# Kernel tuning notes

Hardware: AMD Instinct MI355X
Metric: run time of the kernel (lower is better)

## Reference

```python
import jax, jax.numpy as jnp
import numpy as np

DIM = 2048
N_HEADS = 32
N_KV_HEADS = 8
HEAD_DIM = 64
BATCH = 2
SEQ = 2048
N_REP = N_HEADS // N_KV_HEADS
SCALE = HEAD_DIM ** -0.5
ROPE_BASE = 10000.0


def setup_inputs() -> dict:
    key = jax.random.key(0)
    ks = jax.random.split(key, 5)
    x = jax.random.normal(ks[0], (BATCH, SEQ, DIM), dtype=jnp.float32)
    # weights stored as (in, out) so projection is x @ W
    Wq = jax.random.normal(ks[1], (DIM, N_HEADS * HEAD_DIM), dtype=jnp.float32) * (DIM ** -0.5)
    Wk = jax.random.normal(ks[2], (DIM, N_KV_HEADS * HEAD_DIM), dtype=jnp.float32) * (DIM ** -0.5)
    Wv = jax.random.normal(ks[3], (DIM, N_KV_HEADS * HEAD_DIM), dtype=jnp.float32) * (DIM ** -0.5)
    Wo = jax.random.normal(ks[4], (N_HEADS * HEAD_DIM, DIM), dtype=jnp.float32) * ((N_HEADS * HEAD_DIM) ** -0.5)
    # RoPE tables (seq, head_dim)
    inv_freq = 1.0 / (ROPE_BASE ** (jnp.arange(0, HEAD_DIM, 2, dtype=jnp.float32) / HEAD_DIM))
    t = jnp.arange(SEQ, dtype=jnp.float32)
    freqs = jnp.outer(t, inv_freq)                      # (S, D/2)
    emb = jnp.concatenate([freqs, freqs], axis=-1)      # (S, D)
    cos = jnp.cos(emb)
    sin = jnp.sin(emb)
    # additive causal mask (1,1,S,S)
    neg = jnp.finfo(jnp.float32).min
    causal = jnp.tril(jnp.ones((SEQ, SEQ), dtype=bool))
    attention_mask = jnp.where(causal, 0.0, neg)[None, None, :, :].astype(jnp.float32)
    return {"x": x, "Wq": Wq, "Wk": Wk, "Wv": Wv, "Wo": Wo,
            "cos": cos, "sin": sin, "attention_mask": attention_mask}


def _rotate_half(u):
    h = u.shape[-1] // 2
    return jnp.concatenate([-u[..., h:], u[..., :h]], axis=-1)


def reference(x, Wq, Wk, Wv, Wo, cos, sin, attention_mask):
    b, s, _ = x.shape
    q = (x @ Wq).reshape(b, s, N_HEADS, HEAD_DIM)
    k = (x @ Wk).reshape(b, s, N_KV_HEADS, HEAD_DIM)
    v = (x @ Wv).reshape(b, s, N_KV_HEADS, HEAD_DIM)
    # RoPE, broadcast over head dim (unsqueeze_dim=2)
    c = cos[None, :, None, :]
    sn = sin[None, :, None, :]
    q = q * c + _rotate_half(q) * sn
    k = k * c + _rotate_half(k) * sn
    # repeat KV heads for GQA: (b,s,kvh,d) -> (b,s,h,d)
    k = jnp.repeat(k, N_REP, axis=2)
    v = jnp.repeat(v, N_REP, axis=2)
    # (b,h,s,d)
    q = q.transpose(0, 2, 1, 3)
    k = k.transpose(0, 2, 1, 3)
    v = v.transpose(0, 2, 1, 3)
    scores = jnp.einsum("bhqd,bhkd->bhqk", q, k) * SCALE + attention_mask
    attn = jax.nn.softmax(scores.astype(jnp.float32), axis=-1).astype(q.dtype)
    out = jnp.einsum("bhqk,bhkd->bhqd", attn, v)
    out = out.transpose(0, 2, 1, 3).reshape(b, s, N_HEADS * HEAD_DIM)
    return out @ Wo
```

## Files before the change

### kernel.cpp

```cpp
#include <hip/hip_runtime.h>
#include <hip/hip_bf16.h>

typedef unsigned short u16;
typedef unsigned int   u32;
typedef __bf16 bf16_t;
typedef bf16_t bf16x8 __attribute__((ext_vector_type(8)));
typedef u16    u16x8  __attribute__((ext_vector_type(8)));
typedef float  f32x4  __attribute__((ext_vector_type(4)));

#define DIM  2048
#define SEQ  2048
#define BATCH 2
#define NH   32
#define NKVH 8
#define HD   64
#define KVDIM (NKVH*HD)
#define NQKV (DIM + 2*KVDIM)
#define SCALE 0.125f

__device__ __forceinline__ float b2f(u16 u) {
  union { u32 i; float f; } v; v.i = ((u32)u) << 16; return v.f;
}
__device__ __forceinline__ u16 f2b(float f) {
  union { float f; u32 i; } v; v.f = f;
  u32 x = v.i;
  return (u16)((x + 0x7fffu + ((x >> 16) & 1u)) >> 16);
}
__device__ __forceinline__ u32 pkbf2(float a, float b) {
  __hip_bfloat162 h = __float22bfloat162_rn(float2{a, b});
  union { __hip_bfloat162 h; u32 u; } v; v.h = h; return v.u;
}
__device__ __forceinline__ int probe_bf16(const u32* probe) { return probe[0] != 0u; }
__device__ __forceinline__ float ext_ld(const void* p, long idx, int mode_bf16) {
  return mode_bf16 ? b2f(((const u16*)p)[idx]) : ((const float*)p)[idx];
}
__device__ __forceinline__ f32x4 ld4(const void* p, long idx, int mode_bf16) {
  f32x4 r;
  if (mode_bf16) {
    ushort4 v = *(const ushort4*)((const u16*)p + idx);
    r[0] = b2f(v.x); r[1] = b2f(v.y); r[2] = b2f(v.z); r[3] = b2f(v.w);
  } else {
    float4 v = *(const float4*)((const float*)p + idx);
    r[0] = v.x; r[1] = v.y; r[2] = v.z; r[3] = v.w;
  }
  return r;
}
__device__ __forceinline__ void gload_lds16(const u16* g, u16* l) {
  __builtin_amdgcn_global_load_lds((const __attribute__((address_space(1))) void*)g,
                                   (__attribute__((address_space(3))) void*)l, 16, 0, 0);
}

__global__ void prep(const void* __restrict__ Wq, const void* __restrict__ Wk,
                     const void* __restrict__ Wv, const void* __restrict__ Wo,
                     const void* __restrict__ x, u16* __restrict__ WqkvT,
                     u16* __restrict__ WoT, u16* __restrict__ xb, int use_xb,
                     const u32* __restrict__ probe) {
  int mode = probe_bf16(probe);
  int xt = blockIdx.x;
  int tx = threadIdx.x, ty = threadIdx.y;
  if (xt < 160) {
    __shared__ u16 t[32][33];
    const void* in; int C, c0, obase; u16* out; int ld;
    if (xt < 64)       { in = Wq; C = DIM;   c0 = xt * 32;        obase = 0;           out = WqkvT; ld = DIM; }
    else if (xt < 80)  { in = Wk; C = KVDIM; c0 = (xt - 64) * 32; obase = DIM;         out = WqkvT; ld = DIM; }
    else if (xt < 96)  { in = Wv; C = KVDIM; c0 = (xt - 80) * 32; obase = DIM + KVDIM; out = WqkvT; ld = DIM; }
    else               { in = Wo; C = DIM;   c0 = (xt - 96) * 32; obase = 0;           out = WoT;   ld = DIM; }
    int r0 = blockIdx.y * 32;
#pragma unroll
    for (int i = 0; i < 32; i += 8)
      t[ty + i][tx] = mode ? ((const u16*)in)[(long)(r0 + ty + i) * C + c0 + tx]
                           : f2b(((const float*)in)[(long)(r0 + ty + i) * C + c0 + tx]);
    __syncthreads();
#pragma unroll
    for (int i = 0; i < 32; i += 8)
      out[(long)(obase + c0 + ty + i) * ld + r0 + tx] = t[tx][ty + i];
  } else {
    if (mode || !use_xb) return;
    int tid = ty * 32 + tx;
    long base = ((long)((xt - 160) * 64 + blockIdx.y) * 256 + tid) * 8;
    float4 f0 = *(const float4*)((const float*)x + base);
    float4 f1 = *(const float4*)((const float*)x + base + 4);
    u16x8 t8;
    t8[0] = f2b(f0.x); t8[1] = f2b(f0.y); t8[2] = f2b(f0.z); t8[3] = f2b(f0.w);
    t8[4] = f2b(f1.x); t8[5] = f2b(f1.y); t8[6] = f2b(f1.z); t8[7] = f2b(f1.w);
    *(u16x8*)&xb[base] = t8;
  }
}


__launch_bounds__(256)
__global__ void gemm_qkv(const void* __restrict__ x, const u16* __restrict__ xb,
                         int use_xb, const u16* __restrict__ Bt,
                         u16* __restrict__ Qb, u16* __restrict__ Kb, u16* __restrict__ Vt,
                         const void* __restrict__ cosb, const void* __restrict__ sinb,
                         const u32* __restrict__ probe) {
  int pmode = probe_bf16(probe);
  int mode = (use_xb || pmode) ? 1 : 0;
  const u16* A16 = pmode ? (const u16*)x : xb;
  const float* Af = (const float*)x;
  __shared__ __align__(16) u16 As[128 * 32];
  __shared__ __align__(16) u16 Bs[128 * 32];
  int tid = threadIdx.x, lane = tid & 63, wv = tid >> 6;
  int l16 = lane & 15, q = lane >> 4;
  int bm0 = blockIdx.y * 128, bn0 = blockIdx.x * 128;
  int mbase = (wv & 1) * 64, nbase = (wv >> 1) * 64;
  int c0 = tid, c1 = tid + 256;
  int r0 = c0 >> 2, s0 = (c0 & 3) ^ ((r0 >> 1) & 3);
  int r1 = c1 >> 2, s1 = (c1 & 3) ^ ((r1 >> 1) & 3);
  const int K = DIM;
  long aoff0 = (long)(bm0 + r0) * K + s0 * 8;
  long aoff1 = (long)(bm0 + r1) * K + s1 * 8;
  long boff0 = (long)(bn0 + r0) * K + s0 * 8;
  long boff1 = (long)(bn0 + r1) * K + s1 * 8;
  int rsw = (q ^ ((l16 >> 1) & 3)) * 8;
  f32x4 acc[4][4] = {};

  for (int k0 = 0; k0 < K; k0 += 32) {
    __syncthreads();
    if (mode) {
      gload_lds16(A16 + aoff0 + k0, &As[wv * 512]);
      gload_lds16(A16 + aoff1 + k0, &As[2048 + wv * 512]);
    } else {
      float4 f0 = *(const float4*)(Af + aoff0 + k0);
      float4 f1 = *(const float4*)(Af + aoff0 + k0 + 4);
      u16x8 t;
      t[0] = f2b(f0.x); t[1] = f2b(f0.y); t[2] = f2b(f0.z); t[3] = f2b(f0.w);
      t[4] = f2b(f1.x); t[5] = f2b(f1.y); t[6] = f2b(f1.z); t[7] = f2b(f1.w);
      *(u16x8*)&As[c0 * 8] = t;
      float4 g0 = *(const float4*)(Af + aoff1 + k0);
      float4 g1 = *(const float4*)(Af + aoff1 + k0 + 4);
      u16x8 u;
      u[0] = f2b(g0.x); u[1] = f2b(g0.y); u[2] = f2b(g0.z); u[3] = f2b(g0.w);
      u[4] = f2b(g1.x); u[5] = f2b(g1.y); u[6] = f2b(g1.z); u[7] = f2b(g1.w);
      *(u16x8*)&As[c1 * 8] = u;
    }
    gload_lds16(Bt + boff0 + k0, &Bs[wv * 512]);
    gload_lds16(Bt + boff1 + k0, &Bs[2048 + wv * 512]);
    __syncthreads();
    bf16x8 af[4], bfr[4];
#pragma unroll
    for (int mi = 0; mi < 4; mi++)
      af[mi] = *(const bf16x8*)&As[(mbase + mi * 16 + l16) * 32 + rsw];
#pragma unroll
    for (int ni = 0; ni < 4; ni++)
      bfr[ni] = *(const bf16x8*)&Bs[(nbase + ni * 16 + l16) * 32 + rsw];
#pragma unroll
    for (int mi = 0; mi < 4; mi++)
#pragma unroll
      for (int ni = 0; ni < 4; ni++)
        acc[mi][ni] = __builtin_amdgcn_mfma_f32_16x16x32_bf16(
            bfr[ni], af[mi], acc[mi][ni], 0, 0, 0);
  }

  if (bn0 < DIM + KVDIM) {
    u16* Cb; int ldc, ncol0; float osc;
    if (bn0 < DIM) { Cb = Qb; ldc = DIM; ncol0 = bn0; osc = SCALE; }
    else           { Cb = Kb; ldc = KVDIM; ncol0 = bn0 - DIM; osc = 1.0f; }
#pragma unroll
    for (int mi = 0; mi < 4; mi++) {
      int m = bm0 + mbase + mi * 16 + l16;
      int st = m & (SEQ - 1);
#pragma unroll
      for (int ni = 0; ni < 2; ni++) {
        int dl = ni * 16 + q * 4;
        f32x4 c4 = ld4(cosb, (long)st * HD + dl, pmode);
        f32x4 s4 = ld4(sinb, (long)st * HD + dl, pmode);
        float lo[4], hi[4];
#pragma unroll
        for (int r = 0; r < 4; r++) {
          float a = acc[mi][ni][r], b = acc[mi][ni + 2][r];
          lo[r] = (a * c4[r] - b * s4[r]) * osc;
          hi[r] = (b * c4[r] + a * s4[r]) * osc;
        }
        int n0 = ncol0 + nbase + dl;
        uint2 w0, w1;
        w0.x = pkbf2(lo[0], lo[1]); w0.y = pkbf2(lo[2], lo[3]);
        w1.x = pkbf2(hi[0], hi[1]); w1.y = pkbf2(hi[2], hi[3]);
        *(uint2*)&Cb[(long)m * ldc + n0]      = w0;
        *(uint2*)&Cb[(long)m * ldc + n0 + 32] = w1;
      }
    }
  } else {
    int vcol0 = bn0 - DIM - KVDIM;
#pragma unroll
    for (int mi = 0; mi < 4; mi++) {
      int m = bm0 + mbase + mi * 16 + l16;
      int bb = m >> 11, s = m & (SEQ - 1);
#pragma unroll
      for (int ni = 0; ni < 4; ni++) {
        int vcol = vcol0 + nbase + ni * 16 + q * 4;
        int kvh2 = vcol >> 6, d = vcol & 63;
        long vb = ((long)(bb * NKVH + kvh2) * HD + d) * SEQ + s;
#pragma unroll
        for (int r = 0; r < 4; r++)
          Vt[vb + (long)r * SEQ] = f2b(acc[mi][ni][r]);
      }
    }
  }
}

__launch_bounds__(256)
__global__ void gemm_ao(const u16* __restrict__ A, const u16* __restrict__ Bt,
                        void* __restrict__ C, const u32* __restrict__ probe) {
  int mode = probe_bf16(probe);
  __shared__ __align__(16) u16 As[128 * 32];
  __shared__ __align__(16) u16 Bs[128 * 32];
  int tid = threadIdx.x, lane = tid & 63, wv = tid >> 6;
  int l16 = lane & 15, q = lane >> 4;
  int bm0 = blockIdx.y * 128, bn0 = blockIdx.x * 128;
  int mbase = (wv & 1) * 64, nbase = (wv >> 1) * 64;
  int c0 = tid, c1 = tid + 256;
  int r0 = c0 >> 2, s0 = (c0 & 3) ^ ((r0 >> 1) & 3);
  int r1 = c1 >> 2, s1 = (c1 & 3) ^ ((r1 >> 1) & 3);
  const int K = DIM;
  long aoff0 = (long)(bm0 + r0) * K + s0 * 8;
  long aoff1 = (long)(bm0 + r1) * K + s1 * 8;
  long boff0 = (long)(bn0 + r0) * K + s0 * 8;
  long boff1 = (long)(bn0 + r1) * K + s1 * 8;
  int rsw = (q ^ ((l16 >> 1) & 3)) * 8;
  f32x4 acc[4][4] = {};
  for (int k0 = 0; k0 < K; k0 += 32) {
    __syncthreads();
    gload_lds16(A + aoff0 + k0, &As[wv * 512]);
    gload_lds16(A + aoff1 + k0, &As[2048 + wv * 512]);
    gload_lds16(Bt + boff0 + k0, &Bs[wv * 512]);
    gload_lds16(Bt + boff1 + k0, &Bs[2048 + wv * 512]);
    __syncthreads();
    bf16x8 af[4], bfr[4];
#pragma unroll
    for (int mi = 0; mi < 4; mi++)
      af[mi] = *(const bf16x8*)&As[(mbase + mi * 16 + l16) * 32 + rsw];
#pragma unroll
    for (int ni = 0; ni < 4; ni++)
      bfr[ni] = *(const bf16x8*)&Bs[(nbase + ni * 16 + l16) * 32 + rsw];
#pragma unroll
    for (int mi = 0; mi < 4; mi++)
#pragma unroll
      for (int ni = 0; ni < 4; ni++)
        acc[mi][ni] = __builtin_amdgcn_mfma_f32_16x16x32_bf16(
            bfr[ni], af[mi], acc[mi][ni], 0, 0, 0);
  }
#pragma unroll
  for (int mi = 0; mi < 4; mi++)
#pragma unroll
    for (int ni = 0; ni < 4; ni++) {
      int m = bm0 + mbase + mi * 16 + l16;
      int n0 = bn0 + nbase + ni * 16 + q * 4;
      if (mode) {
        uint2 w;
        w.x = pkbf2(acc[mi][ni][0], acc[mi][ni][1]);
        w.y = pkbf2(acc[mi][ni][2], acc[mi][ni][3]);
        *(uint2*)&((u16*)C)[(long)m * DIM + n0] = w;
      } else {
        float4 f;
        f.x = acc[mi][ni][0]; f.y = acc[mi][ni][1];
        f.z = acc[mi][ni][2]; f.w = acc[mi][ni][3];
        *(float4*)&((float*)C)[(long)m * DIM + n0] = f;
      }
    }
}

__launch_bounds__(256, 2)
__global__ void attn_kernel(const u16* __restrict__ Q, const u16* __restrict__ K,
                            const u16* __restrict__ Vt, u16* __restrict__ AO) {
  __shared__ __align__(16) u16 Ks[2 * 64 * 64];
  __shared__ __align__(16) u16 Vs[2 * 64 * 64];
  __shared__ __align__(16) u16 Ps[4][32 * 64];
  int tid = threadIdx.x, lane = tid & 63, wv = tid >> 6;
  int l16 = lane & 15, q = lane >> 4;
  int i = blockIdx.x;
  int bh = blockIdx.y;
  int b = bh >> 5, h = bh & 31, kvh = h >> 2;
  const u16* Kp = K + (long)b * SEQ * KVDIM + kvh * HD;
  const u16* Vp = Vt + (long)(b * NKVH + kvh) * HD * SEQ;

  int cA = tid, cB = tid + 256;
  int rA = cA >> 3, bA = (cA & 7) ^ (rA & 7);
  int rB = cB >> 3, bB = (cB & 7) ^ (rB & 7);
  const u16* kSrcA = Kp + (long)rA * KVDIM + bA * 8;
  const u16* kSrcB = Kp + (long)rB * KVDIM + bB * 8;
  const u16* vSrcA = Vp + (long)rA * SEQ + bA * 8;
  const u16* vSrcB = Vp + (long)rB * SEQ + bB * 8;
  u16* kDstA = &Ks[(wv * 64 + lane) * 8];
  u16* kDstB = &Ks[(256 + wv * 64 + lane) * 8];
  u16* vDstA = &Vs[(wv * 64 + lane) * 8];
  u16* vDstB = &Vs[(256 + wv * 64 + lane) * 8];

  int e = l16 & 7;
  int off0 = (q ^ e) * 8;
  int off1 = ((4 + q) ^ e) * 8;

  bf16x8 ones;
#pragma unroll
  for (int j = 0; j < 8; j++) ones[j] = (bf16_t)1.0f;

#pragma unroll
  for (int ph = 0; ph < 2; ph++) {
    int t = ph ? (15 - i) : i;
    int qbase = t * 128 + wv * 32;
    const u16* Qp = Q + (long)(b * SEQ + qbase) * DIM + h * HD;
    bf16x8 aq[2][2];
#pragma unroll
    for (int qr = 0; qr < 2; qr++) {
      aq[qr][0] = *(const bf16x8*)&Qp[(qr * 16 + l16) * DIM + q * 8];
      aq[qr][1] = *(const bf16x8*)&Qp[(qr * 16 + l16) * DIM + 32 + q * 8];
    }
    f32x4 o_acc[2][4] = {};
    f32x4 l_acc[2] = {};
    int nkt = 2 * (t + 1);
    int wmax = qbase + 31;

    __syncthreads();
    gload_lds16(kSrcA, kDstA);
    gload_lds16(kSrcB, kDstB);
    gload_lds16(vSrcA, vDstA);
    gload_lds16(vSrcB, vDstB);
    int curo = 0;

    for (int kt = 0; kt < nkt; kt++) {
      __syncthreads();
      if (kt + 1 < nkt) {
        long kk2 = (long)(kt + 1) * 64;
        int nxt = curo ^ 4096;
        gload_lds16(kSrcA + kk2 * KVDIM, kDstA + nxt);
        gload_lds16(kSrcB + kk2 * KVDIM, kDstB + nxt);
        gload_lds16(vSrcA + kk2, vDstA + nxt);
        gload_lds16(vSrcB + kk2, vDstB + nxt);
      }
      int kk = kt * 64;
      if (kk > wmax) { curo ^= 4096; continue; }
      const u16* Ksb = &Ks[curo];
      const u16* Vsb = &Vs[curo];

      bf16x8 bk[4][2], bv[4][2];
#pragma unroll
      for (int ni = 0; ni < 4; ni++) {
        bk[ni][0] = *(const bf16x8*)&Ksb[(ni * 16 + l16) * 64 + off0];
        bk[ni][1] = *(const bf16x8*)&Ksb[(ni * 16 + l16) * 64 + off1];
      }
#pragma unroll
      for (int di = 0; di < 4; di++) {
        bv[di][0] = *(const bf16x8*)&Vsb[(di * 16 + l16) * 64 + off0];
        bv[di][1] = *(const bf16x8*)&Vsb[(di * 16 + l16) * 64 + off1];
      }
      bool diag = (kt >= 2 * t);
#pragma unroll
      for (int qr = 0; qr < 2; qr++) {
        int qb16 = qbase + qr * 16;
        if (kk > qb16 + 15) continue;
        f32x4 sc[4];
#pragma unroll
        for (int ni = 0; ni < 4; ni++) {
          f32x4 z = {};
          z = __builtin_amdgcn_mfma_f32_16x16x32_bf16(bk[ni][0], aq[qr][0], z, 0, 0, 0);
          z = __builtin_amdgcn_mfma_f32_16x16x32_bf16(bk[ni][1], aq[qr][1], z, 0, 0, 0);
          sc[ni] = z;
        }
        int qrow = qb16 + l16;
        if (diag) {
#pragma unroll
          for (int ni = 0; ni < 4; ni++)
#pragma unroll
            for (int r = 0; r < 4; r++) {
              int kv = kk + ni * 16 + q * 4 + r;
              float p = __expf(sc[ni][r]);
              sc[ni][r] = (kv <= qrow) ? p : 0.f;
            }
        } else {
#pragma unroll
          for (int ni = 0; ni < 4; ni++)
#pragma unroll
            for (int r = 0; r < 4; r++) sc[ni][r] = __expf(sc[ni][r]);
        }
#pragma unroll
        for (int ni = 0; ni < 4; ni++) {
          uint2 w;
          w.x = pkbf2(sc[ni][0], sc[ni][1]);
          w.y = pkbf2(sc[ni][2], sc[ni][3]);
          int pblk = (2 * ni + (q >> 1)) ^ e;
          *(uint2*)&Ps[wv][(qr * 16 + l16) * 64 + pblk * 8 + (q & 1) * 4] = w;
        }
        bf16x8 ap0 = *(const bf16x8*)&Ps[wv][(qr * 16 + l16) * 64 + off0];
        bf16x8 ap1 = *(const bf16x8*)&Ps[wv][(qr * 16 + l16) * 64 + off1];
        l_acc[qr] = __builtin_amdgcn_mfma_f32_16x16x32_bf16(ap0, ones, l_acc[qr], 0, 0, 0);
        l_acc[qr] = __builtin_amdgcn_mfma_f32_16x16x32_bf16(ap1, ones, l_acc[qr], 0, 0, 0);
#pragma unroll
        for (int di = 0; di < 4; di++) {
          o_acc[qr][di] = __builtin_amdgcn_mfma_f32_16x16x32_bf16(ap0, bv[di][0], o_acc[qr][di], 0, 0, 0);
          o_acc[qr][di] = __builtin_amdgcn_mfma_f32_16x16x32_bf16(ap1, bv[di][1], o_acc[qr][di], 0, 0, 0);
        }
      }
      curo ^= 4096;
    }
#pragma unroll
    for (int qr = 0; qr < 2; qr++) {
      long obase = (long)(b * SEQ + qbase + qr * 16 + q * 4) * DIM + h * HD;
#pragma unroll
      for (int r = 0; r < 4; r++) {
        float inv = 1.0f / l_acc[qr][r];
#pragma unroll
        for (int di = 0; di < 4; di++)
          AO[obase + (long)r * DIM + di * 16 + l16] = f2b(o_acc[qr][di][r] * inv);
      }
    }
  }
}

extern "C" void kernel_launch(void* const* d_in, const int* in_sizes, int n_in,
                              void* d_out, int out_size, void* d_ws, size_t ws_size,
                              hipStream_t stream) {
  const void* x    = d_in[0];
  const void* Wq   = d_in[1];
  const void* Wk   = d_in[2];
  const void* Wv   = d_in[3];
  const void* Wo   = d_in[4];
  const void* cosb = d_in[5];
  const void* sinb = d_in[6];
  const u32*  probe = (const u32*)d_in[7];

  u16* WqkvT = (u16*)d_ws;
  u16* WoT = WqkvT + (size_t)NQKV * DIM;
  u16* Qb  = WoT + (size_t)DIM * DIM;
  u16* Kb  = Qb  + (size_t)BATCH * SEQ * DIM;
  u16* Vt  = Kb  + (size_t)BATCH * SEQ * KVDIM;
  u16* xb  = Vt  + (size_t)BATCH * NKVH * HD * SEQ;
  u16* AO  = Qb;

  size_t need_xb = ((size_t)(xb - WqkvT) + (size_t)BATCH * SEQ * DIM) * sizeof(u16);
  int use_xb = ws_size >= need_xb;

  int M = BATCH * SEQ;
  prep<<<dim3(224, 64), dim3(32, 8), 0, stream>>>(Wq, Wk, Wv, Wo, x, WqkvT, WoT,
                                                  xb, use_xb, probe);
  gemm_qkv<<<dim3(NQKV / 128, M / 128), 256, 0, stream>>>(x, xb, use_xb, WqkvT,
                                                          Qb, Kb, Vt, cosb, sinb, probe);

  attn_kernel<<<dim3(8, BATCH * NH), 256, 0, stream>>>(Qb, Kb, Vt, AO);

  gemm_ao<<<dim3(DIM / 128, M / 128), 256, 0, stream>>>(AO, WoT, d_out, probe);
}
```

Before: 319.2 us.

## Load K/V tiles directly from global memory per wave, dropping LDS staging and barriers

The attention kernel no longer stages K and V tiles through double-buffered shared memory with block-wide barriers. Each wave now reads its K and V MFMA operands straight from global memory (relying on L1/L2 caching) and exits its key loop early with break instead of continuing to the end. The V loads are placed after the QK MFMAs to overlap latency, and the launch bound's occupancy hint is removed. This removes the barriers and LDS traffic and lets waves run independently, but it costs redundant global/cache reads across the four waves and gives up explicit prefetch.

```diff
diff --git a/kernel.cpp b/kernel.cpp
--- a/kernel.cpp
+++ b/kernel.cpp
@@ -260,11 +260,9 @@
     }
 }
 
-__launch_bounds__(256, 2)
+__launch_bounds__(256)
 __global__ void attn_kernel(const u16* __restrict__ Q, const u16* __restrict__ K,
                             const u16* __restrict__ Vt, u16* __restrict__ AO) {
-  __shared__ __align__(16) u16 Ks[2 * 64 * 64];
-  __shared__ __align__(16) u16 Vs[2 * 64 * 64];
   __shared__ __align__(16) u16 Ps[4][32 * 64];
   int tid = threadIdx.x, lane = tid & 63, wv = tid >> 6;
   int l16 = lane & 15, q = lane >> 4;
@@ -274,18 +272,6 @@
   const u16* Kp = K + (long)b * SEQ * KVDIM + kvh * HD;
   const u16* Vp = Vt + (long)(b * NKVH + kvh) * HD * SEQ;
 
-  int cA = tid, cB = tid + 256;
-  int rA = cA >> 3, bA = (cA & 7) ^ (rA & 7);
-  int rB = cB >> 3, bB = (cB & 7) ^ (rB & 7);
-  const u16* kSrcA = Kp + (long)rA * KVDIM + bA * 8;
-  const u16* kSrcB = Kp + (long)rB * KVDIM + bB * 8;
-  const u16* vSrcA = Vp + (long)rA * SEQ + bA * 8;
-  const u16* vSrcB = Vp + (long)rB * SEQ + bB * 8;
-  u16* kDstA = &Ks[(wv * 64 + lane) * 8];
-  u16* kDstB = &Ks[(256 + wv * 64 + lane) * 8];
-  u16* vDstA = &Vs[(wv * 64 + lane) * 8];
-  u16* vDstB = &Vs[(256 + wv * 64 + lane) * 8];
-
   int e = l16 & 7;
   int off0 = (q ^ e) * 8;
   int off1 = ((4 + q) ^ e) * 8;
@@ -310,52 +296,41 @@
     int nkt = 2 * (t + 1);
     int wmax = qbase + 31;
 
-    __syncthreads();
-    gload_lds16(kSrcA, kDstA);
-    gload_lds16(kSrcB, kDstB);
-    gload_lds16(vSrcA, vDstA);
-    gload_lds16(vSrcB, vDstB);
-    int curo = 0;
-
     for (int kt = 0; kt < nkt; kt++) {
-      __syncthreads();
-      if (kt + 1 < nkt) {
-        long kk2 = (long)(kt + 1) * 64;
-        int nxt = curo ^ 4096;
-        gload_lds16(kSrcA + kk2 * KVDIM, kDstA + nxt);
-        gload_lds16(kSrcB + kk2 * KVDIM, kDstB + nxt);
-        gload_lds16(vSrcA + kk2, vDstA + nxt);
-        gload_lds16(vSrcB + kk2, vDstB + nxt);
-      }
       int kk = kt * 64;
-      if (kk > wmax) { curo ^= 4096; continue; }
-      const u16* Ksb = &Ks[curo];
-      const u16* Vsb = &Vs[curo];
-
-      bf16x8 bk[4][2], bv[4][2];
+      if (kk > wmax) break;
+      bf16x8 bk[4][2];
 #pragma unroll
       for (int ni = 0; ni < 4; ni++) {
-        bk[ni][0] = *(const bf16x8*)&Ksb[(ni * 16 + l16) * 64 + off0];
-        bk[ni][1] = *(const bf16x8*)&Ksb[(ni * 16 + l16) * 64 + off1];
-      }
-#pragma unroll
-      for (int di = 0; di < 4; di++) {
-        bv[di][0] = *(const bf16x8*)&Vsb[(di * 16 + l16) * 64 + off0];
-        bv[di][1] = *(const bf16x8*)&Vsb[(di * 16 + l16) * 64 + off1];
-      }
-      bool diag = (kt >= 2 * t);
+        const u16* kr = Kp + (long)(kk + ni * 16 + l16) * KVDIM;
+        bk[ni][0] = *(const bf16x8*)&kr[q * 8];
+        bk[ni][1] = *(const bf16x8*)&kr[32 + q * 8];
+      }
+      f32x4 sc[2][4];
 #pragma unroll
       for (int qr = 0; qr < 2; qr++) {
         int qb16 = qbase + qr * 16;
         if (kk > qb16 + 15) continue;
-        f32x4 sc[4];
 #pragma unroll
         for (int ni = 0; ni < 4; ni++) {
           f32x4 z = {};
           z = __builtin_amdgcn_mfma_f32_16x16x32_bf16(bk[ni][0], aq[qr][0], z, 0, 0, 0);
           z = __builtin_amdgcn_mfma_f32_16x16x32_bf16(bk[ni][1], aq[qr][1], z, 0, 0, 0);
-          sc[ni] = z;
+          sc[qr][ni] = z;
         }
+      }
+      bf16x8 bv[4][2];
+#pragma unroll
+      for (int di = 0; di < 4; di++) {
+        const u16* vr = Vp + (long)(di * 16 + l16) * SEQ + kk;
+        bv[di][0] = *(const bf16x8*)&vr[q * 8];
+        bv[di][1] = *(const bf16x8*)&vr[32 + q * 8];
+      }
+      bool diag = (kt >= 2 * t);
+#pragma unroll
+      for (int qr = 0; qr < 2; qr++) {
+        int qb16 = qbase + qr * 16;
+        if (kk > qb16 + 15) continue;
         int qrow = qb16 + l16;
         if (diag) {
 #pragma unroll
@@ -363,20 +338,20 @@
 #pragma unroll
             for (int r = 0; r < 4; r++) {
               int kv = kk + ni * 16 + q * 4 + r;
-              float p = __expf(sc[ni][r]);
-              sc[ni][r] = (kv <= qrow) ? p : 0.f;
+              float p = __expf(sc[qr][ni][r]);
+              sc[qr][ni][r] = (kv <= qrow) ? p : 0.f;
             }
         } else {
 #pragma unroll
           for (int ni = 0; ni < 4; ni++)
 #pragma unroll
-            for (int r = 0; r < 4; r++) sc[ni][r] = __expf(sc[ni][r]);
+            for (int r = 0; r < 4; r++) sc[qr][ni][r] = __expf(sc[qr][ni][r]);
         }
 #pragma unroll
         for (int ni = 0; ni < 4; ni++) {
           uint2 w;
-          w.x = pkbf2(sc[ni][0], sc[ni][1]);
-          w.y = pkbf2(sc[ni][2], sc[ni][3]);
+          w.x = pkbf2(sc[qr][ni][0], sc[qr][ni][1]);
+          w.y = pkbf2(sc[qr][ni][2], sc[qr][ni][3]);
           int pblk = (2 * ni + (q >> 1)) ^ e;
           *(uint2*)&Ps[wv][(qr * 16 + l16) * 64 + pblk * 8 + (q & 1) * 4] = w;
         }
@@ -390,7 +365,6 @@
           o_acc[qr][di] = __builtin_amdgcn_mfma_f32_16x16x32_bf16(ap1, bv[di][1], o_acc[qr][di], 0, 0, 0);
         }
       }
-      curo ^= 4096;
     }
 #pragma unroll
     for (int qr = 0; qr < 2; qr++) {
```

After: 386.8 us. 1.21x slower.
